# Kernel tuning notes

Hardware: AMD Instinct MI355X
Metric: run time of the kernel (lower is better)

## Reference

```python
import jax, jax.numpy as jnp
import numpy as np

K, B, ZS, ZH, HS, NF = 32, 4096, 128, 64, 50, 2


def setup_inputs() -> dict:
    key = jax.random.key(0)
    ks = jax.random.split(key, 9)
    s_in = 1.0 / np.sqrt(ZH)   # torch Linear init bound, fan_in = z_half
    s_h = 1.0 / np.sqrt(HS)    # fan_in = hidden
    return {
        "mean": jax.random.normal(ks[0], (B, ZS), dtype=jnp.float32),
        "logvar": 0.1 * jax.random.normal(ks[1], (B, ZS), dtype=jnp.float32),
        "eps": jax.random.normal(ks[2], (K, B, ZS), dtype=jnp.float32),
        "W0": jax.random.uniform(ks[3], (NF, 2, HS, ZH), minval=-s_in, maxval=s_in, dtype=jnp.float32),
        "b0": jax.random.uniform(ks[4], (NF, 2, HS), minval=-s_in, maxval=s_in, dtype=jnp.float32),
        "W1": jax.random.uniform(ks[5], (NF, 2, ZH, HS), minval=-s_h, maxval=s_h, dtype=jnp.float32),
        "b1": jax.random.uniform(ks[6], (NF, 2, ZH), minval=-s_h, maxval=s_h, dtype=jnp.float32),
        "W2": jax.random.uniform(ks[7], (NF, 2, ZH, HS), minval=-s_h, maxval=s_h, dtype=jnp.float32),
        "b2": jax.random.uniform(ks[8], (NF, 2, ZH), minval=-s_h, maxval=s_h, dtype=jnp.float32),
        "k": K,
    }


def _lognormal(z, mean, logvar):
    # log N(z; mean, exp(logvar)), summed over the z dimension -> [k, B]
    d = z.shape[-1]
    return -0.5 * (d * jnp.log(2.0 * jnp.pi)
                   + jnp.sum(logvar + (z - mean) ** 2 * jnp.exp(-logvar), axis=-1))


def reference(mean, logvar, eps, W0, b0, W1, b1, W2, b2, k):
    # reparameterized sample: z ~ N(mean, exp(logvar)), shape [k, B, ZS]
    z = eps * jnp.exp(0.5 * logvar) + mean
    logqz0 = _lognormal(z, mean, logvar)  # [k, B]

    zf = z.reshape(-1, ZS)               # [k*B, ZS]
    z1, z2 = zf[:, :ZH], zf[:, ZH:]
    logdet = jnp.zeros(zf.shape[0], dtype=zf.dtype)

    for i in range(NF):
        # half 0: update z2 conditioned on z1
        h = jnp.tanh(z1 @ W0[i, 0].T + b0[i, 0])        # [k*B, HS]
        mew = h @ W1[i, 0].T + b1[i, 0]                  # [k*B, ZH]
        sig = jax.nn.sigmoid(h @ W2[i, 0].T + b2[i, 0])  # [k*B, ZH]
        z2 = z2 * sig + mew
        logdet = logdet + jnp.sum(jnp.log(sig), axis=1)
        # half 1: update z1 conditioned on z2
        h = jnp.tanh(z2 @ W0[i, 1].T + b0[i, 1])
        mew = h @ W1[i, 1].T + b1[i, 1]
        sig = jax.nn.sigmoid(h @ W2[i, 1].T + b2[i, 1])
        z1 = z1 * sig + mew
        logdet = logdet + jnp.sum(jnp.log(sig), axis=1)

    logdetsum = logdet.reshape(k, -1)                    # [k, B]
    z_out = jnp.concatenate([z1, z2], axis=1).reshape(k, -1, ZS)
    logpz = logqz0 - logdetsum
    return z_out, logpz
```

## Files before the change

### kernel.cpp

```cpp
#include <hip/hip_runtime.h>


typedef unsigned short ushort_t;
typedef unsigned int   uint_t;
typedef short bf8 __attribute__((ext_vector_type(8)));
typedef float f4  __attribute__((ext_vector_type(4)));

#define KK   32
#define BB   4096
#define ZSD  128
#define ZHD  64
#define HSD  50
#define NROWS (KK*BB)

#define WST  72
#define MATS (64*WST)
#define WGL_SHORTS (12*MATS)
#define WS_BYTES   (WGL_SHORTS*2 + 768*4)

__device__ __forceinline__ float bf2f(ushort_t u){ union{uint_t i; float f;} v; v.i = ((uint_t)u)<<16; return v.f; }

__device__ __forceinline__ ushort_t f2bf(float f){
  union{__bf16 h; ushort_t u;} v; v.h = (__bf16)f; return v.u;
}

__device__ __forceinline__ float rcp_fast(float x){ return __builtin_amdgcn_rcpf(x); }

__device__ __forceinline__ float tanh_fast(float x){
  float ax = fabsf(x);
  float t  = __expf(-2.0f*ax);
  float r  = (1.0f - t) * rcp_fast(1.0f + t);
  union{float f; uint_t i;} u, s; u.f = r; s.f = x;
  u.i |= (s.i & 0x80000000u);
  return u.f;
}

__device__ __forceinline__ float sigmoid_fast(float x){
  float ax  = fabsf(x);
  float e   = __expf(-ax);
  float inv = rcp_fast(1.0f + e);
  return (x >= 0.0f) ? inv : e*inv;
}

__device__ __forceinline__ f4 MFMA(bf8 a, bf8 b, f4 c){
  return __builtin_amdgcn_mfma_f32_16x16x32_bf16(a, b, c, 0, 0, 0);
}

__global__ void convert_weights(const float* __restrict__ W0g,
                                const float* __restrict__ b0g,
                                const float* __restrict__ W1g,
                                const float* __restrict__ b1g,
                                const float* __restrict__ W2g,
                                const float* __restrict__ b2g,
                                ushort_t* __restrict__ wgl)
{
  int t = blockIdx.x*256 + threadIdx.x;
  if (t < WGL_SHORTS){
    int mi  = t / MATS;
    int rem = t % MATS;
    int n   = rem / WST;
    int k   = rem % WST;
    int step  = mi / 3;
    int which = mi % 3;
    float v = 0.0f;
    if (which == 0){
      if (n < HSD && k < ZHD) v = W0g[(step*HSD + n)*ZHD + k];
    } else if (which == 1){
      if (k < HSD)            v = W1g[(step*ZHD + n)*HSD + k];
    } else {
      if (k < HSD)            v = W2g[(step*ZHD + n)*HSD + k];
    }
    wgl[t] = f2bf(v);
  }
  if (t < 768){
    float* bp = (float*)(wgl + WGL_SHORTS);
    int step  = t / 192;
    int rem   = t % 192;
    int which = rem / 64;
    int n     = rem % 64;
    float v = 0.0f;
    if (which == 0){ if (n < HSD) v = b0g[step*HSD + n]; }
    else if (which == 1) v = b1g[step*ZHD + n];
    else                 v = b2g[step*ZHD + n];
    bp[t] = v;
  }
}

__device__ __forceinline__ void do_step(
    int s, float (&pz)[2][16], float (&T)[2][4],
    ushort_t* zAw, ushort_t* hAw,
    const ushort_t* wgl, const float* wsb,
    int quad, int l15, int wr)
{
  const ushort_t* ws = wgl + (size_t)(s*3)*MATS;

  bf8 zf[2][2];
  #pragma unroll
  for (int m=0;m<2;++m)
    #pragma unroll
    for (int kt=0;kt<2;++kt)
      zf[m][kt] = *(const bf8*)(zAw + (m*16 + l15)*WST + kt*32 + quad*8);

  #pragma unroll
  for (int nt=0;nt<4;++nt){
    const ushort_t* wb = ws + (0*64 + nt*16 + l15)*WST + quad*8;
    bf8 w0a = *(const bf8*)(wb);
    bf8 w0b = *(const bf8*)(wb + 32);
    float b0v = wsb[(s*3+0)*64 + nt*16 + l15];
    #pragma unroll
    for (int m=0;m<2;++m){
      f4 acc = {0.f,0.f,0.f,0.f};
      acc = MFMA(zf[m][0], w0a, acc);
      acc = MFMA(zf[m][1], w0b, acc);
      #pragma unroll
      for (int i=0;i<4;++i){
        float h = tanh_fast(acc[i] + b0v);
        hAw[(m*16 + quad*4 + i)*WST + nt*16 + l15] = f2bf(h);
      }
    }
  }

  bf8 hf[2][2];
  #pragma unroll
  for (int m=0;m<2;++m)
    #pragma unroll
    for (int kt=0;kt<2;++kt)
      hf[m][kt] = *(const bf8*)(hAw + (m*16 + l15)*WST + kt*32 + quad*8);

  float sp[2][4];
  #pragma unroll
  for (int m=0;m<2;++m)
    #pragma unroll
    for (int i=0;i<4;++i) sp[m][i] = 1.0f;

  #pragma unroll
  for (int nt=0;nt<4;++nt){
    const ushort_t* w1p = ws + (1*64 + nt*16 + l15)*WST + quad*8;
    const ushort_t* w2p = ws + (2*64 + nt*16 + l15)*WST + quad*8;
    bf8 w1a = *(const bf8*)(w1p);
    bf8 w1b = *(const bf8*)(w1p + 32);
    bf8 w2a = *(const bf8*)(w2p);
    bf8 w2b = *(const bf8*)(w2p + 32);
    float b1v = wsb[(s*3+1)*64 + nt*16 + l15];
    float b2v = wsb[(s*3+2)*64 + nt*16 + l15];
    #pragma unroll
    for (int m=0;m<2;++m){
      f4 am = {0.f,0.f,0.f,0.f};
      f4 as = {0.f,0.f,0.f,0.f};
      am = MFMA(hf[m][0], w1a, am);
      am = MFMA(hf[m][1], w1b, am);
      as = MFMA(hf[m][0], w2a, as);
      as = MFMA(hf[m][1], w2b, as);
      #pragma unroll
      for (int i=0;i<4;++i){
        float mew  = am[i] + b1v;
        float spre = as[i] + b2v;
        float sig  = sigmoid_fast(spre);
        sp[m][i] *= sig;
        pz[m][nt*4+i] = fmaf(pz[m][nt*4+i], sig, mew);
      }
    }
  }

  #pragma unroll
  for (int m=0;m<2;++m)
    #pragma unroll
    for (int i=0;i<4;++i)
      T[m][i] += __logf(sp[m][i]);

  if (wr){
    #pragma unroll
    for (int m=0;m<2;++m)
      #pragma unroll
      for (int nt=0;nt<4;++nt)
        #pragma unroll
        for (int i=0;i<4;++i)
          zAw[(m*16 + quad*4 + i)*WST + nt*16 + l15] = f2bf(pz[m][nt*4+i]);
  }
}

__global__ __launch_bounds__(128) void flow_mfma(
    const float* __restrict__ mean, const float* __restrict__ logvar,
    const float* __restrict__ eps,
    const ushort_t* __restrict__ wgl,
    float* __restrict__ out)
{
  __shared__ __align__(16) ushort_t zA[2][32*WST];
  __shared__ __align__(16) ushort_t hA[2][32*WST];

  const int tid  = threadIdx.x;
  const int wave = tid >> 6;
  const int lane = tid & 63;
  const int quad = lane >> 4;
  const int l15  = lane & 15;
  const int rbase = blockIdx.x*64 + wave*32;

  const float* wsb = (const float*)(wgl + WGL_SHORTS);
  ushort_t* zAw = zA[wave];
  ushort_t* hAw = hA[wave];

  float z1D[2][16], z2D[2][16];
  float T[2][4];

  #pragma unroll
  for (int m=0;m<2;++m){
    #pragma unroll
    for (int i=0;i<4;++i){
      int rrow = rbase + m*16 + quad*4 + i;
      int brow = rrow & (BB-1);
      const float* er = eps    + (size_t)rrow*ZSD;
      const float* mr = mean   + (size_t)brow*ZSD;
      const float* vr = logvar + (size_t)brow*ZSD;
      float acc = 0.f;
      #pragma unroll
      for (int nt=0;nt<4;++nt){
        int c1 = nt*16 + l15;
        int c2 = 64 + c1;
        float e1 = er[c1], v1 = vr[c1], m1 = mr[c1];
        float e2 = er[c2], v2 = vr[c2], m2 = mr[c2];
        z1D[m][nt*4+i] = fmaf(e1, __expf(0.5f*v1), m1);
        z2D[m][nt*4+i] = fmaf(e2, __expf(0.5f*v2), m2);
        acc += (v1 + e1*e1) + (v2 + e2*e2);
      }
      T[m][i] = 0.5f*acc;
    }
  }

  #pragma unroll
  for (int m=0;m<2;++m)
    #pragma unroll
    for (int nt=0;nt<4;++nt)
      #pragma unroll
      for (int i=0;i<4;++i)
        zAw[(m*16 + quad*4 + i)*WST + nt*16 + l15] = f2bf(z1D[m][nt*4+i]);

  #pragma unroll 1
  for (int it=0; it<2; ++it){
    do_step(2*it+0, z2D, T, zAw, hAw, wgl, wsb, quad, l15, 1);
    do_step(2*it+1, z1D, T, zAw, hAw, wgl, wsb, quad, l15, it==0);
  }

  #pragma unroll
  for (int m=0;m<2;++m){
    #pragma unroll
    for (int i=0;i<4;++i){
      int rrow = rbase + m*16 + quad*4 + i;
      float* orow = out + (size_t)rrow*ZSD;
      #pragma unroll
      for (int nt=0;nt<4;++nt){
        orow[nt*16 + l15]      = z1D[m][nt*4+i];
        orow[64 + nt*16 + l15] = z2D[m][nt*4+i];
      }
    }
  }

  #pragma unroll
  for (int m=0;m<2;++m)
    #pragma unroll
    for (int i=0;i<4;++i){
      float v = T[m][i];
      v += __shfl_xor(v, 1, 64);
      v += __shfl_xor(v, 2, 64);
      v += __shfl_xor(v, 4, 64);
      v += __shfl_xor(v, 8, 64);
      T[m][i] = v;
    }
  if (l15 == 0){
    const float NC = -0.5f * 128.0f * 1.8378770664093453f;
    #pragma unroll
    for (int m=0;m<2;++m)
      #pragma unroll
      for (int i=0;i<4;++i){
        int rrow = rbase + m*16 + quad*4 + i;
        out[(size_t)NROWS*ZSD + rrow] = NC - T[m][i];
      }
  }
}

extern "C" void kernel_launch(void* const* d_in, const int* in_sizes, int n_in,
                              void* d_out, int out_size, void* d_ws, size_t ws_size,
                              hipStream_t stream)
{
  const float* mean   = (const float*)d_in[0];
  const float* logvar = (const float*)d_in[1];
  const float* eps    = (const float*)d_in[2];
  const float* W0     = (const float*)d_in[3];
  const float* b0     = (const float*)d_in[4];
  const float* W1     = (const float*)d_in[5];
  const float* b1     = (const float*)d_in[6];
  const float* W2     = (const float*)d_in[7];
  const float* b2     = (const float*)d_in[8];
  ushort_t* wgl = (ushort_t*)d_ws;

  convert_weights<<<(WGL_SHORTS + 255)/256, 256, 0, stream>>>(W0,b0,W1,b1,W2,b2, wgl);
  flow_mfma<<<NROWS/64, 128, 0, stream>>>(mean, logvar, eps, wgl, (float*)d_out);
}
```

Baseline: 174.8 us.

## Transpose MFMA operands so each lane owns rows, enabling vectorized loads and stores

Swaps the A/B operands of every MFMA so the accumulator holds a row's features across four consecutive columns per lane instead of four rows per lane. Global eps/mean/logvar reads and output writes become 16-byte vector accesses, bias reads become f4 loads, and LDS writes of h and z become packed 8-byte stores instead of scalar 2-byte stores. The row-sum reduction for logdet now needs only two cross-lane shuffles. The change is meant to cut memory-instruction count and improve coalescing, but each lane now reads a contiguous row chunk, so global access patterns change and LDS bank conflicts may shift.

After: 184.1 us. 1.05x slower.

```diff
diff --git a/kernel.cpp b/kernel.cpp
--- a/kernel.cpp
+++ b/kernel.cpp
@@ -22,6 +22,13 @@
 
 __device__ __forceinline__ ushort_t f2bf(float f){
   union{__bf16 h; ushort_t u;} v; v.h = (__bf16)f; return v.u;
+}
+
+__device__ __forceinline__ uint2 pack4(float a, float b, float c, float d){
+  uint2 r;
+  r.x = (uint_t)f2bf(a) | ((uint_t)f2bf(b) << 16);
+  r.y = (uint_t)f2bf(c) | ((uint_t)f2bf(d) << 16);
+  return r;
 }
 
 __device__ __forceinline__ float rcp_fast(float x){ return __builtin_amdgcn_rcpf(x); }
@@ -87,95 +94,96 @@
 }
 
 __device__ __forceinline__ void do_step(
-    int s, float (&pz)[2][16], float (&T)[2][4],
+    int s, float (&pz)[2][16], float (&T)[2],
     ushort_t* zAw, ushort_t* hAw,
     const ushort_t* wgl, const float* wsb,
     int quad, int l15, int wr)
 {
   const ushort_t* ws = wgl + (size_t)(s*3)*MATS;
+  const float* bp0 = wsb + (s*3+0)*64;
+  const float* bp1 = wsb + (s*3+1)*64;
+  const float* bp2 = wsb + (s*3+2)*64;
+  const int qc = quad*4;
 
   bf8 zf[2][2];
   #pragma unroll
-  for (int m=0;m<2;++m)
+  for (int t=0;t<2;++t)
     #pragma unroll
     for (int kt=0;kt<2;++kt)
-      zf[m][kt] = *(const bf8*)(zAw + (m*16 + l15)*WST + kt*32 + quad*8);
-
+      zf[t][kt] = *(const bf8*)(zAw + (t*16 + l15)*WST + kt*32 + quad*8);
+
+  float hrow[2][16];
   #pragma unroll
   for (int nt=0;nt<4;++nt){
     const ushort_t* wb = ws + (0*64 + nt*16 + l15)*WST + quad*8;
-    bf8 w0a = *(const bf8*)(wb);
-    bf8 w0b = *(const bf8*)(wb + 32);
-    float b0v = wsb[(s*3+0)*64 + nt*16 + l15];
-    #pragma unroll
-    for (int m=0;m<2;++m){
+    bf8 a0  = *(const bf8*)(wb);
+    bf8 a0b = *(const bf8*)(wb + 32);
+    f4 b0v  = *(const f4*)(bp0 + nt*16 + qc);
+    #pragma unroll
+    for (int t=0;t<2;++t){
       f4 acc = {0.f,0.f,0.f,0.f};
-      acc = MFMA(zf[m][0], w0a, acc);
-      acc = MFMA(zf[m][1], w0b, acc);
-      #pragma unroll
-      for (int i=0;i<4;++i){
-        float h = tanh_fast(acc[i] + b0v);
-        hAw[(m*16 + quad*4 + i)*WST + nt*16 + l15] = f2bf(h);
-      }
-    }
-  }
+      acc = MFMA(a0,  zf[t][0], acc);
+      acc = MFMA(a0b, zf[t][1], acc);
+      #pragma unroll
+      for (int i=0;i<4;++i)
+        hrow[t][nt*4+i] = tanh_fast(acc[i] + b0v[i]);
+    }
+  }
+
+  #pragma unroll
+  for (int t=0;t<2;++t)
+    #pragma unroll
+    for (int nt=0;nt<4;++nt)
+      *(uint2*)(hAw + (t*16 + l15)*WST + nt*16 + qc) =
+        pack4(hrow[t][nt*4+0], hrow[t][nt*4+1], hrow[t][nt*4+2], hrow[t][nt*4+3]);
 
   bf8 hf[2][2];
   #pragma unroll
-  for (int m=0;m<2;++m)
+  for (int t=0;t<2;++t)
     #pragma unroll
     for (int kt=0;kt<2;++kt)
-      hf[m][kt] = *(const bf8*)(hAw + (m*16 + l15)*WST + kt*32 + quad*8);
-
-  float sp[2][4];
-  #pragma unroll
-  for (int m=0;m<2;++m)
-    #pragma unroll
-    for (int i=0;i<4;++i) sp[m][i] = 1.0f;
-
+      hf[t][kt] = *(const bf8*)(hAw + (t*16 + l15)*WST + kt*32 + quad*8);
+
+  float spa[2] = {1.0f, 1.0f}, spb[2] = {1.0f, 1.0f};
   #pragma unroll
   for (int nt=0;nt<4;++nt){
     const ushort_t* w1p = ws + (1*64 + nt*16 + l15)*WST + quad*8;
     const ushort_t* w2p = ws + (2*64 + nt*16 + l15)*WST + quad*8;
-    bf8 w1a = *(const bf8*)(w1p);
-    bf8 w1b = *(const bf8*)(w1p + 32);
-    bf8 w2a = *(const bf8*)(w2p);
-    bf8 w2b = *(const bf8*)(w2p + 32);
-    float b1v = wsb[(s*3+1)*64 + nt*16 + l15];
-    float b2v = wsb[(s*3+2)*64 + nt*16 + l15];
-    #pragma unroll
-    for (int m=0;m<2;++m){
+    bf8 a1  = *(const bf8*)(w1p);
+    bf8 a1b = *(const bf8*)(w1p + 32);
+    bf8 a2  = *(const bf8*)(w2p);
+    bf8 a2b = *(const bf8*)(w2p + 32);
+    f4 b1v = *(const f4*)(bp1 + nt*16 + qc);
+    f4 b2v = *(const f4*)(bp2 + nt*16 + qc);
+    #pragma unroll
+    for (int t=0;t<2;++t){
       f4 am = {0.f,0.f,0.f,0.f};
       f4 as = {0.f,0.f,0.f,0.f};
-      am = MFMA(hf[m][0], w1a, am);
-      am = MFMA(hf[m][1], w1b, am);
-      as = MFMA(hf[m][0], w2a, as);
-      as = MFMA(hf[m][1], w2b, as);
+      am = MFMA(a1,  hf[t][0], am);
+      am = MFMA(a1b, hf[t][1], am);
+      as = MFMA(a2,  hf[t][0], as);
+      as = MFMA(a2b, hf[t][1], as);
       #pragma unroll
       for (int i=0;i<4;++i){
-        float mew  = am[i] + b1v;
-        float spre = as[i] + b2v;
+        float mew  = am[i] + b1v[i];
+        float spre = as[i] + b2v[i];
         float sig  = sigmoid_fast(spre);
-        sp[m][i] *= sig;
-        pz[m][nt*4+i] = fmaf(pz[m][nt*4+i], sig, mew);
+        if (nt < 2) spa[t] *= sig; else spb[t] *= sig;
+        pz[t][nt*4+i] = fmaf(pz[t][nt*4+i], sig, mew);
       }
     }
   }
-
-  #pragma unroll
-  for (int m=0;m<2;++m)
-    #pragma unroll
-    for (int i=0;i<4;++i)
-      T[m][i] += __logf(sp[m][i]);
+  #pragma unroll
+  for (int t=0;t<2;++t)
+    T[t] += __logf(spa[t]) + __logf(spb[t]);
 
   if (wr){
     #pragma unroll
-    for (int m=0;m<2;++m)
+    for (int t=0;t<2;++t)
       #pragma unroll
       for (int nt=0;nt<4;++nt)
-        #pragma unroll
-        for (int i=0;i<4;++i)
-          zAw[(m*16 + quad*4 + i)*WST + nt*16 + l15] = f2bf(pz[m][nt*4+i]);
+        *(uint2*)(zAw + (t*16 + l15)*WST + nt*16 + qc) =
+          pack4(pz[t][nt*4+0], pz[t][nt*4+1], pz[t][nt*4+2], pz[t][nt*4+3]);
   }
 }
 
@@ -193,6 +201,7 @@
   const int lane = tid & 63;
   const int quad = lane >> 4;
   const int l15  = lane & 15;
+  const int qc   = quad*4;
   const int rbase = blockIdx.x*64 + wave*32;
 
   const float* wsb = (const float*)(wgl + WGL_SHORTS);
@@ -200,39 +209,38 @@
   ushort_t* hAw = hA[wave];
 
   float z1D[2][16], z2D[2][16];
-  float T[2][4];
-
-  #pragma unroll
-  for (int m=0;m<2;++m){
-    #pragma unroll
-    for (int i=0;i<4;++i){
-      int rrow = rbase + m*16 + quad*4 + i;
-      int brow = rrow & (BB-1);
-      const float* er = eps    + (size_t)rrow*ZSD;
-      const float* mr = mean   + (size_t)brow*ZSD;
-      const float* vr = logvar + (size_t)brow*ZSD;
-      float acc = 0.f;
-      #pragma unroll
-      for (int nt=0;nt<4;++nt){
-        int c1 = nt*16 + l15;
-        int c2 = 64 + c1;
-        float e1 = er[c1], v1 = vr[c1], m1 = mr[c1];
-        float e2 = er[c2], v2 = vr[c2], m2 = mr[c2];
-        z1D[m][nt*4+i] = fmaf(e1, __expf(0.5f*v1), m1);
-        z2D[m][nt*4+i] = fmaf(e2, __expf(0.5f*v2), m2);
-        acc += (v1 + e1*e1) + (v2 + e2*e2);
+  float T[2];
+
+  #pragma unroll
+  for (int t=0;t<2;++t){
+    int rrow = rbase + t*16 + l15;
+    int brow = rrow & (BB-1);
+    const float* er = eps    + (size_t)rrow*ZSD;
+    const float* mr = mean   + (size_t)brow*ZSD;
+    const float* vr = logvar + (size_t)brow*ZSD;
+    float acc = 0.f;
+    #pragma unroll
+    for (int nt=0;nt<4;++nt){
+      int c1 = nt*16 + qc;
+      int c2 = 64 + c1;
+      f4 e1 = *(const f4*)(er + c1), v1 = *(const f4*)(vr + c1), m1 = *(const f4*)(mr + c1);
+      f4 e2 = *(const f4*)(er + c2), v2 = *(const f4*)(vr + c2), m2 = *(const f4*)(mr + c2);
+      #pragma unroll
+      for (int i=0;i<4;++i){
+        z1D[t][nt*4+i] = fmaf(e1[i], __expf(0.5f*v1[i]), m1[i]);
+        z2D[t][nt*4+i] = fmaf(e2[i], __expf(0.5f*v2[i]), m2[i]);
+        acc += (v1[i] + e1[i]*e1[i]) + (v2[i] + e2[i]*e2[i]);
       }
-      T[m][i] = 0.5f*acc;
-    }
-  }
-
-  #pragma unroll
-  for (int m=0;m<2;++m)
+    }
+    T[t] = 0.5f*acc;
+  }
+
+  #pragma unroll
+  for (int t=0;t<2;++t)
     #pragma unroll
     for (int nt=0;nt<4;++nt)
-      #pragma unroll
-      for (int i=0;i<4;++i)
-        zAw[(m*16 + quad*4 + i)*WST + nt*16 + l15] = f2bf(z1D[m][nt*4+i]);
+      *(uint2*)(zAw + (t*16 + l15)*WST + nt*16 + qc) =
+        pack4(z1D[t][nt*4+0], z1D[t][nt*4+1], z1D[t][nt*4+2], z1D[t][nt*4+3]);
 
   #pragma unroll 1
   for (int it=0; it<2; ++it){
@@ -241,39 +249,30 @@
   }
 
   #pragma unroll
-  for (int m=0;m<2;++m){
-    #pragma unroll
-    for (int i=0;i<4;++i){
-      int rrow = rbase + m*16 + quad*4 + i;
-      float* orow = out + (size_t)rrow*ZSD;
-      #pragma unroll
-      for (int nt=0;nt<4;++nt){
-        orow[nt*16 + l15]      = z1D[m][nt*4+i];
-        orow[64 + nt*16 + l15] = z2D[m][nt*4+i];
-      }
-    }
-  }
-
-  #pragma unroll
-  for (int m=0;m<2;++m)
-    #pragma unroll
-    for (int i=0;i<4;++i){
-      float v = T[m][i];
-      v += __shfl_xor(v, 1, 64);
-      v += __shfl_xor(v, 2, 64);
-      v += __shfl_xor(v, 4, 64);
-      v += __shfl_xor(v, 8, 64);
-      T[m][i] = v;
-    }
-  if (l15 == 0){
+  for (int t=0;t<2;++t){
+    int rrow = rbase + t*16 + l15;
+    float* orow = out + (size_t)rrow*ZSD;
+    #pragma unroll
+    for (int nt=0;nt<4;++nt){
+      f4 o1 = {z1D[t][nt*4+0], z1D[t][nt*4+1], z1D[t][nt*4+2], z1D[t][nt*4+3]};
+      f4 o2 = {z2D[t][nt*4+0], z2D[t][nt*4+1], z2D[t][nt*4+2], z2D[t][nt*4+3]};
+      *(f4*)(orow + nt*16 + qc)      = o1;
+      *(f4*)(orow + 64 + nt*16 + qc) = o2;
+    }
+  }
+
+  #pragma unroll
+  for (int t=0;t<2;++t){
+    float v = T[t];
+    v += __shfl_xor(v, 16, 64);
+    v += __shfl_xor(v, 32, 64);
+    T[t] = v;
+  }
+  if (lane < 16){
     const float NC = -0.5f * 128.0f * 1.8378770664093453f;
     #pragma unroll
-    for (int m=0;m<2;++m)
-      #pragma unroll
-      for (int i=0;i<4;++i){
-        int rrow = rbase + m*16 + quad*4 + i;
-        out[(size_t)NROWS*ZSD + rrow] = NC - T[m][i];
-      }
+    for (int t=0;t<2;++t)
+      out[(size_t)NROWS*ZSD + rbase + t*16 + l15] = NC - T[t];
   }
 }
 
```
